# Kernel tuning notes

Measured on AMD Instinct MI355X. Metric: run time of the kernel, lower is better.

## Reference

```python
import jax, jax.numpy as jnp
import numpy as np


def setup_inputs() -> dict:
    key = jax.random.key(0)
    ks = jax.random.split(key, 4)
    B, C, H, W, L = 2, 32, 128, 128, 7
    return {
        "x": jax.random.normal(ks[0], (B, C, H, W), jnp.float32),
        # conv3d3x3: Conv3d(C, 32, (1,3,3)) -> 2D conv weight [32, C, 3, 3]
        "w1": jax.random.normal(ks[1], (32, C, 3, 3), jnp.float32) * 0.05,
        "b1": jnp.zeros((32,), jnp.float32),
        # conv3d1x1: Conv3d(32, 1, 1) -> pointwise weight [1, 32]
        "w2": jax.random.normal(ks[2], (1, 32), jnp.float32) * 0.05,
        "b2": jnp.zeros((1,), jnp.float32),
        # conv3d9x9x1: Conv3d(C, C, (1,L,L)) -> weight [C, C, L, L]
        "w3": jax.random.normal(ks[3], (C, C, L, L), jnp.float32) * 0.02,
        "b3": jnp.zeros((C,), jnp.float32),
        "local_scale": 7,
    }


def reference(x, w1, b1, w2, b2, w3, b3, local_scale):
    # sliding_window branch of Local_attention.forward
    L = int(local_scale)
    pad = L // 2
    B, C, H, W = x.shape
    P = H * W
    # F.unfold with kernel (H, W) and padding=pad over padded input gives the
    # L*L shifted copies of the full feature map. Equivalent gather:
    # local_x[b,c,ki*W+kj,wi,wj] = x_pad[b,c, ki+wi, kj+wj]
    xp = jnp.pad(x, ((0, 0), (0, 0), (pad, pad), (pad, pad)))
    local = jnp.stack(
        [xp[:, :, wi:wi + H, wj:wj + W] for wi in range(L) for wj in range(L)],
        axis=-1,
    )  # [B, C, H, W, L*L]
    local = local.reshape(B, C, P, L, L)
    # Conv3d kernels with depth-size 1 act independently per depth slice ->
    # fold the depth (pixel) dim into the batch and run 2D convs.
    lx = local.transpose(0, 2, 1, 3, 4).reshape(B * P, C, L, L)
    k = jax.lax.conv_general_dilated(
        lx, w1, window_strides=(1, 1), padding=((1, 1), (1, 1)),
        dimension_numbers=("NCHW", "OIHW", "NCHW"),
    ) + b1[None, :, None, None]                      # [B*P, 32, L, L]
    att = jax.nn.sigmoid(
        jnp.einsum("nchw,oc->nohw", k, w2) + b2[None, :, None, None]
    )                                                # [B*P, 1, L, L]
    att_x = lx * att + lx                            # gated residual
    # Conv3d(C, C, (1,L,L)) valid -> full contraction over (C_in, L, L)
    out = jnp.einsum("nchw,ochw->no", att_x, w3) + b3  # [B*P, C]
    output = out.reshape(B, P, C).transpose(0, 2, 1).reshape(B, C, H, W)
    att_mp = att.reshape(B, P, 1, L, L).transpose(0, 2, 1, 3, 4)  # [B,1,P,L,L]
    return output, att_mp
```

## Files before the change

### kernel.cpp

```cpp
#include <hip/hip_runtime.h>

typedef __attribute__((ext_vector_type(8))) short bf16x8;
typedef __attribute__((ext_vector_type(4))) float f32x4;
typedef __attribute__((ext_vector_type(4))) unsigned int u32x4;
typedef __attribute__((ext_vector_type(2))) unsigned int u32x2;

namespace {
constexpr int OUT0 = 2 * 32 * 16384;
}

__device__ __forceinline__ unsigned int bf16_rne(float f) {
  unsigned int u = __builtin_bit_cast(unsigned int, f);
  return u + 0x7fffu + ((u >> 16) & 1u);
}
__device__ __forceinline__ unsigned int bf16_rhu(float f) {
  return __builtin_bit_cast(unsigned int, f) + 0x8000u;
}
__device__ __forceinline__ unsigned int pack_rne(float lo, float hi) {
  return __builtin_amdgcn_perm(bf16_rne(hi), bf16_rne(lo), 0x07060302u);
}
__device__ __forceinline__ unsigned int pack_rhu(float lo, float hi) {
  return __builtin_amdgcn_perm(bf16_rhu(hi), bf16_rhu(lo), 0x07060302u);
}
__device__ __forceinline__ float bf16_to_f32(unsigned int u16v) {
  return __builtin_bit_cast(float, u16v << 16);
}

__global__ __launch_bounds__(256) void prep_kernel(
    const float* __restrict__ w1, const float* __restrict__ b1,
    const float* __restrict__ w2, const float* __restrict__ b2,
    const float* __restrict__ w3,
    float* __restrict__ wk, unsigned int* __restrict__ w3f) {
  int t = threadIdx.x, blk = blockIdx.x;
  if (blk < 98) {
    int f = blk * 256 + t;
    int d = f & 3;
    int lane = (f >> 2) & 63;
    int nt = (f >> 8) & 1;
    int ij = f >> 9;
    int o = nt * 16 + (lane & 15);
    int k0 = ((lane >> 4) << 3) + 2 * d;
    float f0 = w3[o * 1568 + k0 * 49 + ij];
    float f1 = w3[o * 1568 + (k0 + 1) * 49 + ij];
    w3f[f] = pack_rne(f0, f1);
  } else {
    int k = (blk - 98) * 256 + t;
    if (k < 288) {
      int c = k / 9, r = k - c * 9;
      float s = 0.f;
#pragma unroll
      for (int o = 0; o < 32; ++o) s += w2[o] * w1[o * 288 + c * 9 + r];
      wk[k] = s;
    } else if (k == 288) {
      float s = b2[0];
#pragma unroll
      for (int o = 0; o < 32; ++o) s += w2[o] * b1[o];
      wk[288] = s;
    }
  }
}

__global__ __launch_bounds__(512, 4) void fused_kernel(
    const float* __restrict__ x, const float* __restrict__ wk,
    const unsigned int* __restrict__ w3f, const float* __restrict__ b3,
    float* __restrict__ out, float* __restrict__ att_out) {
  __shared__ __align__(16) char regA[16384];
  unsigned short* xs16 = (unsigned short*)regA;
  float* as_ = (float*)regA;
  __shared__ __align__(16) unsigned short xh[224 * 40];
  __shared__ unsigned short ysb[9 * 224];
  __shared__ float wks[289];

  int t = threadIdx.x;
  int bi = blockIdx.x;
  int b = bi >> 8;
  int tile = bi & 255;
  int y0 = (tile >> 4) << 3, x0 = (tile & 15) << 3;
  const float* xb = x + ((long)b << 19);

  for (int k = t; k < 289; k += 512) wks[k] = wk[k];

#pragma unroll
  for (int it = 0; it < 4; ++it) {
    int idx = it * 512 + t;
    int c = idx >> 6;
    int r64 = idx & 63;
    int row = r64 >> 2, seg = r64 & 3;
    int gy = y0 + row - 4;
    int gxs = x0 + (seg << 2) - 4;
    f32x4 v = {0.f, 0.f, 0.f, 0.f};
    if ((unsigned)gy < 128u && (unsigned)gxs < 128u)
      v = *reinterpret_cast<const f32x4*>(xb + (c << 14) + (gy << 7) + gxs);
    u32x2 p;
    p[0] = pack_rhu(v[0], v[1]);
    p[1] = pack_rhu(v[2], v[3]);
    *reinterpret_cast<u32x2*>(reinterpret_cast<unsigned int*>(xs16) +
                              (c << 7) + (r64 << 1)) = p;
  }
  __syncthreads();

  if (t < 256) {
    int r = t >> 4;
    bool inner = (unsigned)(r - 1) < 14u;
    int n = t - 16;
    unsigned int u[32];
#pragma unroll
    for (int c = 0; c < 32; ++c) u[c] = xs16[(c << 8) + t];
    float s[9];
#pragma unroll
    for (int dd = 0; dd < 9; ++dd) s[dd] = 0.f;
#pragma unroll
    for (int c = 0; c < 32; ++c) {
      float xf = bf16_to_f32(u[c]);
#pragma unroll
      for (int dd = 0; dd < 9; ++dd) s[dd] += xf * wks[c * 9 + dd];
    }
    if (inner) {
#pragma unroll
      for (int dd = 0; dd < 9; ++dd)
        ysb[dd * 224 + n] = (unsigned short)(bf16_rhu(s[dd]) >> 16);
      unsigned int* xhd = reinterpret_cast<unsigned int*>(xh) + n * 20;
#pragma unroll
      for (int g4 = 0; g4 < 4; ++g4) {
        u32x4 d;
#pragma unroll
        for (int e = 0; e < 4; ++e) {
          int k2 = g4 * 4 + e;
          d[e] = __builtin_amdgcn_perm(u[2 * k2 + 1], u[2 * k2], 0x05040100u);
        }
        *reinterpret_cast<u32x4*>(xhd + g4 * 4) = d;
      }
    }
  }
  __syncthreads();

#pragma unroll 1
  for (int it = 0; it < 7; ++it) {
    int f = it * 512 + t;
    if (f < 3136) {
      int pos = f >> 6;
      int px = f & 63;
      int py = px >> 3, pxl = px & 7;
      int i = pos / 7, j = pos - i * 7;
      float s = wks[288];
#pragma unroll
      for (int di = 0; di < 3; ++di) {
        int ii = i + di - 1;
        if ((unsigned)ii >= 7u) continue;
#pragma unroll
        for (int dj = 0; dj < 3; ++dj) {
          int jj = j + dj - 1;
          if ((unsigned)jj >= 7u) continue;
          s += bf16_to_f32(
              (unsigned int)ysb[(di * 3 + dj) * 224 + (py + ii) * 16 + pxl + jj + 1]);
        }
      }
      float e = __expf(-s);
      as_[pos * 68 + px] = 1.f + __builtin_amdgcn_rcpf(1.f + e);
    }
  }
  __syncthreads();

#pragma unroll 1
  for (int it = 0; it < 7; ++it) {
    int f = it * 512 + t;
    if (f < 3136) {
      int row = f / 392;
      int rem = f - row * 392;
      int pxl = rem / 49;
      int pos = rem - pxl * 49;
      long base = ((long)(b << 14) + ((y0 + row) << 7) + x0) * 49;
      att_out[base + rem] = as_[pos * 68 + (row << 3) + pxl] - 1.f;
    }
  }

  int wv = t >> 6, lane = t & 63;
  int mt = wv >> 1, th = wv & 1;
  int ml = lane & 15, q = lane >> 4;
  int px = mt * 16 + ml;
  int py = px >> 3, pxl = px & 7;
  f32x4 acc0 = {0.f, 0.f, 0.f, 0.f};
  f32x4 acc1 = {0.f, 0.f, 0.f, 0.f};
  const u32x4* bp = reinterpret_cast<const u32x4*>(w3f) + lane;
  auto tap = [&](int ij) {
    int i = (ij * 37) >> 8;
    int j = ij - i * 7;
    int nb = (py + i) * 16 + pxl + 1 + j;
    u32x4 bw0 = bp[ij * 128];
    u32x4 bw1 = bp[ij * 128 + 64];
    bf16x8 af = *reinterpret_cast<const bf16x8*>(&xh[nb * 40 + (q << 3)]);
    f32x4 gv = *reinterpret_cast<const f32x4*>(&as_[ij * 68 + mt * 16 + (q << 2)]);
    f32x4 z = {0.f, 0.f, 0.f, 0.f};
    f32x4 P0 = __builtin_amdgcn_mfma_f32_16x16x32_bf16(
        af, __builtin_bit_cast(bf16x8, bw0), z, 0, 0, 0);
    f32x4 P1 = __builtin_amdgcn_mfma_f32_16x16x32_bf16(
        af, __builtin_bit_cast(bf16x8, bw1), z, 0, 0, 0);
#pragma unroll
    for (int r = 0; r < 4; ++r) {
      acc0[r] += gv[r] * P0[r];
      acc1[r] += gv[r] * P1[r];
    }
  };
  if (th == 0) {
#pragma unroll 3
    for (int k = 0; k < 25; ++k) tap(2 * k);
  } else {
#pragma unroll 3
    for (int k = 0; k < 24; ++k) tap(2 * k + 1);
  }
  __syncthreads();

  {
    int o0 = ml, o1 = 16 + ml;
    int base = mt * 16 + (q << 2);
    if (th == 0) {
      float bv0 = b3[o0], bv1 = b3[o1];
#pragma unroll
      for (int r = 0; r < 4; ++r) {
        as_[o0 * 68 + base + r] = acc0[r] + bv0;
        as_[o1 * 68 + base + r] = acc1[r] + bv1;
      }
    }
    __syncthreads();
    if (th == 1) {
#pragma unroll
      for (int r = 0; r < 4; ++r) {
        as_[o0 * 68 + base + r] += acc0[r];
        as_[o1 * 68 + base + r] += acc1[r];
      }
    }
  }
  __syncthreads();
#pragma unroll
  for (int rep = 0; rep < 4; ++rep) {
    int idx = rep * 512 + t;
    int o = idx >> 6, pxs = idx & 63;
    out[((long)b << 19) + (o << 14) + ((y0 + (pxs >> 3)) << 7) + x0 + (pxs & 7)]
        = as_[o * 68 + pxs];
  }
}

extern "C" void kernel_launch(void* const* d_in, const int* in_sizes, int n_in,
                              void* d_out, int out_size, void* d_ws, size_t ws_size,
                              hipStream_t stream) {
  const float* x  = (const float*)d_in[0];
  const float* w1 = (const float*)d_in[1];
  const float* b1 = (const float*)d_in[2];
  const float* w2 = (const float*)d_in[3];
  const float* b2 = (const float*)d_in[4];
  const float* w3 = (const float*)d_in[5];
  const float* b3 = (const float*)d_in[6];

  float* out = (float*)d_out;
  float* att_out = out + OUT0;
  float* wk = (float*)d_ws;
  unsigned int* w3f = (unsigned int*)((char*)d_ws + 4096);

  prep_kernel<<<100, 256, 0, stream>>>(w1, b1, w2, b2, w3, wk, w3f);
  fused_kernel<<<512, 512, 0, stream>>>(x, wk, w3f, b3, out, att_out);
}
```

Before: 90.05 us.

## Split 3x3 pre-conv across all waves, pad ysb rows, prefetch w3 taps

```diff
diff --git a/kernel.cpp b/kernel.cpp
--- a/kernel.cpp
+++ b/kernel.cpp
@@ -68,7 +68,7 @@
   unsigned short* xs16 = (unsigned short*)regA;
   float* as_ = (float*)regA;
   __shared__ __align__(16) unsigned short xh[224 * 40];
-  __shared__ unsigned short ysb[9 * 224];
+  __shared__ unsigned short ysb[9 * 238];
   __shared__ float wks[289];
 
   int t = threadIdx.x;
@@ -77,6 +77,15 @@
   int tile = bi & 255;
   int y0 = (tile >> 4) << 3, x0 = (tile & 15) << 3;
   const float* xb = x + ((long)b << 19);
+
+  int wv = t >> 6, lane = t & 63;
+  int mt = wv >> 1, th = wv & 1;
+  int ml = lane & 15, q = lane >> 4;
+  const u32x4* bp = reinterpret_cast<const u32x4*>(w3f) + lane;
+  u32x4 pw0 = bp[th * 128];
+  u32x4 pw1 = bp[th * 128 + 64];
+  u32x4 pw2 = bp[(th + 2) * 128];
+  u32x4 pw3 = bp[(th + 2) * 128 + 64];
 
   for (int k = t; k < 289; k += 512) wks[k] = wk[k];
 
@@ -99,36 +108,56 @@
   }
   __syncthreads();
 
-  if (t < 256) {
-    int r = t >> 4;
+  {
+    int p = t & 255;
+    bool hi = t >= 256;
+    int r = p >> 4;
     bool inner = (unsigned)(r - 1) < 14u;
-    int n = t - 16;
+    int n = p - 16;
+    int n17 = n + (n >> 4);
     unsigned int u[32];
 #pragma unroll
-    for (int c = 0; c < 32; ++c) u[c] = xs16[(c << 8) + t];
-    float s[9];
-#pragma unroll
-    for (int dd = 0; dd < 9; ++dd) s[dd] = 0.f;
-#pragma unroll
-    for (int c = 0; c < 32; ++c) {
-      float xf = bf16_to_f32(u[c]);
-#pragma unroll
-      for (int dd = 0; dd < 9; ++dd) s[dd] += xf * wks[c * 9 + dd];
-    }
-    if (inner) {
-#pragma unroll
-      for (int dd = 0; dd < 9; ++dd)
-        ysb[dd * 224 + n] = (unsigned short)(bf16_rhu(s[dd]) >> 16);
-      unsigned int* xhd = reinterpret_cast<unsigned int*>(xh) + n * 20;
-#pragma unroll
-      for (int g4 = 0; g4 < 4; ++g4) {
-        u32x4 d;
-#pragma unroll
-        for (int e = 0; e < 4; ++e) {
-          int k2 = g4 * 4 + e;
-          d[e] = __builtin_amdgcn_perm(u[2 * k2 + 1], u[2 * k2], 0x05040100u);
+    for (int c = 0; c < 32; ++c) u[c] = xs16[(c << 8) + p];
+    if (!hi) {
+      float s[4];
+#pragma unroll
+      for (int dd = 0; dd < 4; ++dd) s[dd] = 0.f;
+#pragma unroll
+      for (int c = 0; c < 32; ++c) {
+        float xf = bf16_to_f32(u[c]);
+#pragma unroll
+        for (int dd = 0; dd < 4; ++dd) s[dd] += xf * wks[c * 9 + dd];
+      }
+      if (inner) {
+#pragma unroll
+        for (int dd = 0; dd < 4; ++dd)
+          ysb[dd * 238 + n17] = (unsigned short)(bf16_rhu(s[dd]) >> 16);
+        unsigned int* xhd = reinterpret_cast<unsigned int*>(xh) + n * 20;
+#pragma unroll
+        for (int g4 = 0; g4 < 4; ++g4) {
+          u32x4 d;
+#pragma unroll
+          for (int e = 0; e < 4; ++e) {
+            int k2 = g4 * 4 + e;
+            d[e] = __builtin_amdgcn_perm(u[2 * k2 + 1], u[2 * k2], 0x05040100u);
+          }
+          *reinterpret_cast<u32x4*>(xhd + g4 * 4) = d;
         }
-        *reinterpret_cast<u32x4*>(xhd + g4 * 4) = d;
+      }
+    } else {
+      float s[5];
+#pragma unroll
+      for (int dd = 0; dd < 5; ++dd) s[dd] = 0.f;
+#pragma unroll
+      for (int c = 0; c < 32; ++c) {
+        float xf = bf16_to_f32(u[c]);
+#pragma unroll
+        for (int dd = 0; dd < 5; ++dd) s[dd] += xf * wks[c * 9 + 4 + dd];
+      }
+      if (inner) {
+#pragma unroll
+        for (int dd = 0; dd < 5; ++dd)
+          ysb[(4 + dd) * 238 + n17] = (unsigned short)(bf16_rhu(s[dd]) >> 16);
       }
     }
   }
@@ -152,7 +181,7 @@
           int jj = j + dj - 1;
           if ((unsigned)jj >= 7u) continue;
           s += bf16_to_f32(
-              (unsigned int)ysb[(di * 3 + dj) * 224 + (py + ii) * 16 + pxl + jj + 1]);
+              (unsigned int)ysb[(di * 3 + dj) * 238 + (py + ii) * 17 + pxl + jj + 1]);
         }
       }
       float e = __expf(-s);
@@ -174,23 +203,18 @@
     }
   }
 
-  int wv = t >> 6, lane = t & 63;
-  int mt = wv >> 1, th = wv & 1;
-  int ml = lane & 15, q = lane >> 4;
   int px = mt * 16 + ml;
   int py = px >> 3, pxl = px & 7;
   f32x4 acc0 = {0.f, 0.f, 0.f, 0.f};
   f32x4 acc1 = {0.f, 0.f, 0.f, 0.f};
-  const u32x4* bp = reinterpret_cast<const u32x4*>(w3f) + lane;
-  auto tap = [&](int ij) {
+  auto tapw = [&](int ij, u32x4 bw0, u32x4 bw1) {
     int i = (ij * 37) >> 8;
     int j = ij - i * 7;
     int nb = (py + i) * 16 + pxl + 1 + j;
-    u32x4 bw0 = bp[ij * 128];
-    u32x4 bw1 = bp[ij * 128 + 64];
     bf16x8 af = *reinterpret_cast<const bf16x8*>(&xh[nb * 40 + (q << 3)]);
     f32x4 gv = *reinterpret_cast<const f32x4*>(&as_[ij * 68 + mt * 16 + (q << 2)]);
     f32x4 z = {0.f, 0.f, 0.f, 0.f};
+    __builtin_amdgcn_s_setprio(1);
     f32x4 P0 = __builtin_amdgcn_mfma_f32_16x16x32_bf16(
         af, __builtin_bit_cast(bf16x8, bw0), z, 0, 0, 0);
     f32x4 P1 = __builtin_amdgcn_mfma_f32_16x16x32_bf16(
@@ -200,13 +224,17 @@
       acc0[r] += gv[r] * P0[r];
       acc1[r] += gv[r] * P1[r];
     }
+    __builtin_amdgcn_s_setprio(0);
   };
+  auto tap = [&](int ij) { tapw(ij, bp[ij * 128], bp[ij * 128 + 64]); };
+  tapw(th, pw0, pw1);
+  tapw(th + 2, pw2, pw3);
   if (th == 0) {
 #pragma unroll 3
-    for (int k = 0; k < 25; ++k) tap(2 * k);
+    for (int k = 2; k < 25; ++k) tap(2 * k);
   } else {
 #pragma unroll 3
-    for (int k = 0; k < 24; ++k) tap(2 * k + 1);
+    for (int k = 2; k < 24; ++k) tap(2 * k + 1);
   }
   __syncthreads();
 
```

Result: slower. 125.5 us (+39.4%).
